# Performance work log

Measured on AMD Instinct MI355X. Metric: run time of the kernel, lower is better.

Reference implementation:

```python
import jax, jax.numpy as jnp
import numpy as np

EPS_NORM = 1e-12   # F.normalize eps
EPS_W = 1e-8       # weight eps in knn


def _l2_normalize(x):
    n = jnp.linalg.norm(x, axis=-1, keepdims=True)
    return x / jnp.maximum(n, EPS_NORM)


def setup_inputs() -> dict:
    key = jax.random.key(0)
    k1, k2, k3 = jax.random.split(key, 3)
    B, N, D, T = 2048, 100000, 128, 8
    return {
        "query": jax.random.normal(k1, (B, D), dtype=jnp.float32),
        "supports": jax.random.normal(k2, (N, D), dtype=jnp.float32),
        "targets": jax.random.uniform(k3, (N, T), dtype=jnp.float32),
        "k": 16,
    }


def reference(query, supports, targets, k):
    q = _l2_normalize(query)           # [B, D]
    s = _l2_normalize(supports)        # [N, D]
    dists = 1.0 - q @ s.T              # [B, N] cosine distance
    k = min(k, dists.shape[-1])
    # smallest-k distances == largest-k of negated distances
    neg_d, idx = jax.lax.top_k(-dists, k)   # [B, k]
    d = -neg_d
    w = 1.0 / (d + EPS_W)
    w = w / jnp.sum(w, axis=-1, keepdims=True)          # [B, k]
    tv = targets[idx]                                    # [B, k, T] gather
    return jnp.sum(tv * w[..., None], axis=1)            # [B, T]
```

## Files before the change

kernel.cpp:

```cpp
#include <hip/hip_runtime.h>


#define NSLICES 64
#define CN 64
#define BQ 128
#define NSUB 50
#define NGS (NSLICES * NSUB)
#define QCAP 64
#define THR_MARGIN 0.013f

typedef __bf16 bf16x8 __attribute__((ext_vector_type(8)));
typedef float f32x16 __attribute__((ext_vector_type(16)));

__device__ __forceinline__ ushort f2bf_rne(float f) {
  unsigned u = __float_as_uint(f);
  return (ushort)((u + 0x7FFFu + ((u >> 16) & 1u)) >> 16);
}
__device__ __forceinline__ ushort f2bf_down(float f) {
  unsigned u = __float_as_uint(f);
  return (ushort)((u >> 16) + (u >> 31));
}
__device__ __forceinline__ unsigned bf2key(ushort b) {
  return (unsigned)(b ^ ((b & 0x8000u) ? 0xFFFFu : 0x8000u));
}

__device__ __forceinline__ void bitonic64(float& v, unsigned& i, int lane) {
  #pragma unroll
  for (int k = 2; k <= 64; k <<= 1) {
    #pragma unroll
    for (int j = k >> 1; j > 0; j >>= 1) {
      float pv = __shfl_xor(v, j);
      unsigned pi = (unsigned)__shfl_xor((int)i, j);
      bool up = ((lane & k) == 0);
      bool lower = ((lane & j) == 0);
      bool gt = (v > pv) || (v == pv && i > pi);
      bool keep = (up == lower) ? !gt : gt;
      if (!keep) { v = pv; i = pi; }
    }
  }
}

__global__ __launch_bounds__(256) void norm_rows_k(
    const float* __restrict__ sup, const float* __restrict__ qry,
    ushort* __restrict__ sb, ushort* __restrict__ qb, int N, int nq) {
  int row = blockIdx.x * 4 + (threadIdx.x >> 6);
  int lane = threadIdx.x & 63;
  if (row >= N + nq) return;
  const float* src = (row < N) ? (sup + (size_t)row * 128)
                               : (qry + (size_t)(row - N) * 128);
  ushort* dst = (row < N) ? (sb + (size_t)row * 128)
                          : (qb + (size_t)(row - N) * 128);
  float2 v = *reinterpret_cast<const float2*>(src + lane * 2);
  float ss = v.x * v.x + v.y * v.y;
  #pragma unroll
  for (int o = 1; o < 64; o <<= 1) ss += __shfl_xor(ss, o);
  float inv = 1.0f / fmaxf(sqrtf(ss), 1e-12f);
  ushort2 h = make_ushort2(f2bf_rne(v.x * inv), f2bf_rne(v.y * inv));
  *reinterpret_cast<ushort2*>(dst + lane * 2) = h;
}

__device__ __forceinline__ void stage_lin(const ushort* __restrict__ sn,
                                          ushort* dst, int cb, int s1, int tid) {
  #pragma unroll
  for (int r = 0; r < 4; ++r) {
    int o = (r << 12) + tid * 16;
    int row = o >> 8;
    int dj = (o >> 4) & 15;
    int sj = dj ^ (row & 15);
    int srow = min(cb + row, s1 - 1);
    __builtin_amdgcn_global_load_lds(
        (const unsigned int*)(sn + (size_t)srow * 128 + sj * 8),
        (unsigned int*)(dst + (o >> 1)), 16, 0, 0);
  }
}

__device__ __forceinline__ void stage_list(const ushort* __restrict__ sn,
                                           ushort* dst, const ushort* slist_b,
                                           int s0, int s1, int tid) {
  #pragma unroll
  for (int r = 0; r < 4; ++r) {
    int o = (r << 12) + tid * 16;
    int row = o >> 8;
    int dj = (o >> 4) & 15;
    int sj = dj ^ (row & 15);
    int sub = slist_b[row >> 5];
    int lrow = (sub == 0xFFFF) ? 0 : sub * 32 + (row & 31);
    int srow = min(s0 + lrow, s1 - 1);
    __builtin_amdgcn_global_load_lds(
        (const unsigned int*)(sn + (size_t)srow * 128 + sj * 8),
        (unsigned int*)(dst + (o >> 1)), 16, 0, 0);
  }
}

__global__ __launch_bounds__(256, 4) void pass1_k(
    const ushort* __restrict__ qn, const ushort* __restrict__ sn,
    ushort* __restrict__ cm, int N) {
  __shared__ ushort st[2][CN * 128];
  const int tid = threadIdx.x;
  const int w = tid >> 6, lane = tid & 63;
  const int q32 = lane & 31, half = lane >> 5;
  const int L = blockIdx.x;
  const int xcd = L & 7, i6 = L >> 3;
  const int qtile = i6 & 15;
  const int slice = (xcd << 3) | (i6 >> 4);
  const int qbase = qtile * BQ;
  const int SLICE = (N + NSLICES - 1) / NSLICES;
  const int s0 = slice * SLICE;
  const int s1 = min(N, s0 + SLICE);
  const int nch = (s1 - s0 + CN - 1) / CN;

  stage_lin(sn, &st[0][0], s0, s1, tid);

  bf16x8 afr[8];
  {
    const int qrow = qbase + w * 32 + q32;
    #pragma unroll
    for (int t = 0; t < 8; ++t)
      afr[t] = *reinterpret_cast<const bf16x8*>(qn + (size_t)qrow * 128 + t * 16 + half * 8);
  }
  __syncthreads();

  int buf = 0;
  for (int ch = 0; ch < nch; ++ch) {
    const int cb = s0 + ch * CN;
    if (ch + 1 < nch) stage_lin(sn, &st[buf ^ 1][0], cb + CN, s1, tid);
    const ushort* stc = &st[buf][0];
    const bool lastch = (ch == nch - 1);

    f32x16 a0 = {0.f}, a1 = {0.f};
    #pragma unroll
    for (int r = 1; r < 16; ++r) { a0[r] = 0.f; a1[r] = 0.f; }
    const int r0 = q32;
    #pragma unroll
    for (int t = 0; t < 8; ++t) {
      int jb = t * 2 + half;
      int cj0 = jb ^ (r0 & 15);
      int cj1 = jb ^ ((r0 + 32) & 15);
      bf16x8 s0 = *reinterpret_cast<const bf16x8*>(&stc[r0 * 128 + cj0 * 8]);
      bf16x8 s1 = *reinterpret_cast<const bf16x8*>(&stc[(r0 + 32) * 128 + cj1 * 8]);
      a0 = __builtin_amdgcn_mfma_f32_32x32x16_bf16(s0, afr[t], a0, 0, 0, 0);
      a1 = __builtin_amdgcn_mfma_f32_32x32x16_bf16(s1, afr[t], a1, 0, 0, 0);
    }
    float v0 = -3.0e38f, v1 = -3.0e38f;
    if (lastch) {
      #pragma unroll
      for (int r = 0; r < 16; ++r) {
        int row = (r & 3) + 8 * (r >> 2) + (half << 2);
        if (cb + row < s1) v0 = fmaxf(v0, a0[r]);
        if (cb + 32 + row < s1) v1 = fmaxf(v1, a1[r]);
      }
    } else {
      #pragma unroll
      for (int r = 0; r < 16; ++r) {
        v0 = fmaxf(v0, a0[r]);
        v1 = fmaxf(v1, a1[r]);
      }
    }
    v0 = fmaxf(v0, __shfl_xor(v0, 32));
    v1 = fmaxf(v1, __shfl_xor(v1, 32));
    if (lane < 32) {
      int q = qbase + w * 32 + q32;
      size_t e0 = ((size_t)(q >> 2) * NGS + slice * NSUB + ch * 2) * 4 + (q & 3);
      cm[e0] = f2bf_down(v0);
      cm[e0 + 4] = f2bf_down(v1);
    }
    __syncthreads();
    buf ^= 1;
  }

  const int miss = NSUB - nch * 2;
  for (int idx = tid; idx < miss * BQ; idx += 256) {
    int sub = nch * 2 + idx / BQ;
    int q = qbase + (idx % BQ);
    cm[((size_t)(q >> 2) * NGS + (size_t)(slice * NSUB + sub)) * 4 + (q & 3)] = 0xFF80;
  }
}

__global__ __launch_bounds__(256) void thr_k(const ushort* __restrict__ cm,
                                             float* __restrict__ thr,
                                             unsigned* __restrict__ cnt) {
  const int q = blockIdx.x * 4 + (threadIdx.x >> 6);
  const int lane = threadIdx.x & 63;
  const size_t base = (size_t)(q >> 2) * NGS * 4 + (q & 3);
  unsigned keys[NGS / 128];
  #pragma unroll
  for (int j = 0; j < NGS / 128; ++j) {
    unsigned k0 = bf2key(cm[base + (size_t)(lane + 128 * j) * 4]);
    unsigned k1 = bf2key(cm[base + (size_t)(lane + 64 + 128 * j) * 4]);
    keys[j] = k0 | (k1 << 16);
  }
  unsigned res = 0;
  for (int b = 15; b >= 0; --b) {
    unsigned t = res | (1u << b);
    int c = 0;
    #pragma unroll
    for (int j = 0; j < NGS / 128; ++j)
      c += (int)((keys[j] & 0xFFFFu) >= t) + (int)((keys[j] >> 16) >= t);
    #pragma unroll
    for (int o = 1; o < 64; o <<= 1) c += __shfl_xor(c, o);
    if (c >= 16) res = t;
  }
  if (lane == 0) {
    ushort b16 = (ushort)((res & 0x8000u) ? (res ^ 0x8000u) : (res ^ 0xFFFFu));
    thr[q] = __uint_as_float((unsigned)b16 << 16) - THR_MARGIN;
    cnt[q] = 0;
  }
}

__global__ __launch_bounds__(256, 4) void pass2_k(
    const ushort* __restrict__ qn, const ushort* __restrict__ sn,
    const ushort* __restrict__ cm, const float* __restrict__ thr,
    unsigned* __restrict__ cnt, float2* __restrict__ candq, int N) {
  __shared__ ushort st[2][CN * 128];
  __shared__ float thr_l[BQ];
  __shared__ unsigned char hit[NSUB];
  __shared__ ushort slist[NSUB + 2];
  __shared__ int nhit_s;

  const int tid = threadIdx.x;
  const int w = tid >> 6, lane = tid & 63;
  const int q32 = lane & 31, half = lane >> 5;
  const int L = blockIdx.x;
  const int xcd = L & 7, i6 = L >> 3;
  const int qtile = i6 & 15;
  const int slice = (xcd << 3) | (i6 >> 4);
  const int qbase = qtile * BQ;
  const int SLICE = (N + NSLICES - 1) / NSLICES;
  const int s0 = slice * SLICE;
  const int s1 = min(N, s0 + SLICE);
  const int slen = s1 - s0;

  if (tid < BQ) thr_l[tid] = thr[qbase + tid];
  if (tid < NSUB) hit[tid] = 0;
  __syncthreads();

  {
    int q = qbase + (tid & 127);
    int sh = tid >> 7;
    float tq = thr_l[tid & 127];
    size_t base = (size_t)(q >> 2) * NGS * 4 + (q & 3);
    for (int j = 0; j < NSUB / 2; ++j) {
      int s = 2 * j + sh;
      ushort b = cm[base + (size_t)(slice * NSUB + s) * 4];
      if (__uint_as_float((unsigned)b << 16) >= tq) hit[s] = 1;
    }
  }
  __syncthreads();
  if (tid < 64) {
    bool f = (tid < NSUB) && hit[tid];
    unsigned long long bm = __ballot(f);
    int pos = __popcll(bm & ((1ull << tid) - 1ull));
    if (f) slist[pos] = (ushort)tid;
    if (tid == 0) {
      int total = __popcll(bm);
      nhit_s = total;
      slist[total] = 0xFFFF;
      slist[total + 1] = 0xFFFF;
    }
  }
  __syncthreads();
  const int nhit = nhit_s;
  if (nhit == 0) return;
  const int nb = (nhit + 1) >> 1;

  bf16x8 afr[8];
  {
    const int qrow = qbase + w * 32 + q32;
    #pragma unroll
    for (int t = 0; t < 8; ++t)
      afr[t] = *reinterpret_cast<const bf16x8*>(qn + (size_t)qrow * 128 + t * 16 + half * 8);
  }
  const float thrq = thr_l[w * 32 + q32];

  stage_list(sn, &st[0][0], &slist[0], s0, s1, tid);
  __syncthreads();

  int buf = 0;
  for (int b = 0; b < nb; ++b) {
    if (b + 1 < nb) stage_list(sn, &st[buf ^ 1][0], &slist[(b + 1) * 2], s0, s1, tid);
    const ushort* stc = &st[buf][0];

    f32x16 a0 = {0.f}, a1 = {0.f};
    #pragma unroll
    for (int r = 1; r < 16; ++r) { a0[r] = 0.f; a1[r] = 0.f; }
    const int r0 = q32;
    #pragma unroll
    for (int t = 0; t < 8; ++t) {
      int jb = t * 2 + half;
      int cj = jb ^ (r0 & 15);
      bf16x8 sf0 = *reinterpret_cast<const bf16x8*>(&stc[r0 * 128 + cj * 8]);
      bf16x8 sf1 = *reinterpret_cast<const bf16x8*>(&stc[(r0 + 32) * 128 + cj * 8]);
      a0 = __builtin_amdgcn_mfma_f32_32x32x16_bf16(sf0, afr[t], a0, 0, 0, 0);
      a1 = __builtin_amdgcn_mfma_f32_32x32x16_bf16(sf1, afr[t], a1, 0, 0, 0);
    }
    const int subA = slist[b * 2], subB = slist[b * 2 + 1];
    const int q = qbase + w * 32 + q32;
    if (subA != 0xFFFF) {
      unsigned hm = 0;
      #pragma unroll
      for (int r = 0; r < 16; ++r) {
        int row = (r & 3) + 8 * (r >> 2) + (half << 2);
        if (subA * 32 + row < slen && a0[r] >= thrq) hm |= 1u << r;
      }
      if (__any(hm != 0u)) {
        #pragma unroll
        for (int r = 0; r < 16; ++r) {
          if (hm & (1u << r)) {
            int row = (r & 3) + 8 * (r >> 2) + (half << 2);
            unsigned p = atomicAdd(&cnt[q], 1u);
            if (p < (unsigned)QCAP)
              candq[(size_t)q * QCAP + p] =
                  make_float2(a0[r], __int_as_float(s0 + subA * 32 + row));
          }
        }
      }
    }
    if (subB != 0xFFFF) {
      unsigned hm = 0;
      #pragma unroll
      for (int r = 0; r < 16; ++r) {
        int row = (r & 3) + 8 * (r >> 2) + (half << 2);
        if (subB * 32 + row < slen && a1[r] >= thrq) hm |= 1u << r;
      }
      if (__any(hm != 0u)) {
        #pragma unroll
        for (int r = 0; r < 16; ++r) {
          if (hm & (1u << r)) {
            int row = (r & 3) + 8 * (r >> 2) + (half << 2);
            unsigned p = atomicAdd(&cnt[q], 1u);
            if (p < (unsigned)QCAP)
              candq[(size_t)q * QCAP + p] =
                  make_float2(a1[r], __int_as_float(s0 + subB * 32 + row));
          }
        }
      }
    }
    __syncthreads();
    buf ^= 1;
  }
}

__global__ __launch_bounds__(256) void merge_refine_k(
    const float* __restrict__ query, const float* __restrict__ supports,
    const float* __restrict__ targets, const unsigned* __restrict__ cnt,
    const float2* __restrict__ candq, float* __restrict__ out) {
  const int W = threadIdx.x >> 6;
  const int q = blockIdx.x * 4 + W;
  const int lane = threadIdx.x & 63;
  __shared__ float qh_s[4][128];
  __shared__ float2 list[4][QCAP];
  __shared__ float2 refd[4][QCAP];

  int total = min((int)cnt[q], QCAP);
  if (lane < total) list[W][lane] = candq[(size_t)q * QCAP + lane];

  float2 qv = *reinterpret_cast<const float2*>(query + (size_t)q * 128 + lane * 2);
  double qss = (double)qv.x * qv.x + (double)qv.y * qv.y;
  #pragma unroll
  for (int o = 1; o < 64; o <<= 1) qss += __shfl_xor(qss, o);
  float qn1 = fmaxf((float)sqrt(qss), 1e-12f);
  qh_s[W][lane * 2] = qv.x / qn1;
  qh_s[W][lane * 2 + 1] = qv.y / qn1;
  __syncthreads();

  const int g16 = lane >> 4, m16 = lane & 15;
  float qh[8];
  #pragma unroll
  for (int d = 0; d < 8; ++d) qh[d] = qh_s[W][m16 * 8 + d];
  int rounds = (total + 3) >> 2;
  for (int r = 0; r < rounds; ++r) {
    int cc = r * 4 + g16;
    bool valid = cc < total;
    float2 ce = valid ? list[W][cc] : make_float2(0.f, __int_as_float(0));
    int sidx = __float_as_int(ce.y);
    float4 sa = *reinterpret_cast<const float4*>(supports + (size_t)sidx * 128 + m16 * 8);
    float4 sb = *reinterpret_cast<const float4*>(supports + (size_t)sidx * 128 + m16 * 8 + 4);
    float sv[8] = {sa.x, sa.y, sa.z, sa.w, sb.x, sb.y, sb.z, sb.w};
    double ss = 0.0, dt = 0.0;
    #pragma unroll
    for (int d = 0; d < 8; ++d) {
      ss += (double)sv[d] * sv[d];
      dt += (double)qh[d] * sv[d];
    }
    #pragma unroll
    for (int o = 1; o < 16; o <<= 1) {
      ss += __shfl_xor(ss, o);
      dt += __shfl_xor(dt, o);
    }
    if (m16 == 0 && valid) {
      float sn1 = fmaxf((float)sqrt(ss), 1e-12f);
      refd[W][cc] = make_float2((float)(1.0 - dt / (double)sn1), ce.y);
    }
  }
  __syncthreads();

  float dv = (lane < total) ? refd[W][lane].x : 3.0e38f;
  unsigned di = (lane < total) ? (unsigned)__float_as_int(refd[W][lane].y) : 0xFFFFFFFFu;
  bitonic64(dv, di, lane);

  float wv = (lane < 16) ? 1.0f / (dv + 1e-8f) : 0.0f;
  float wsum = wv;
  #pragma unroll
  for (int o = 1; o < 64; o <<= 1) wsum += __shfl_xor(wsum, o);
  float acc[8];
  #pragma unroll
  for (int t = 0; t < 8; ++t) acc[t] = 0.f;
  if (lane < 16) {
    float wn = wv / wsum;
    const float* tp = targets + (size_t)di * 8;
    #pragma unroll
    for (int t = 0; t < 8; ++t) acc[t] = wn * tp[t];
  }
  #pragma unroll
  for (int o = 1; o < 16; o <<= 1) {
    #pragma unroll
    for (int t = 0; t < 8; ++t) acc[t] += __shfl_xor(acc[t], o);
  }
  if (lane == 0) {
    #pragma unroll
    for (int t = 0; t < 8; ++t) out[(size_t)q * 8 + t] = acc[t];
  }
}

extern "C" void kernel_launch(void* const* d_in, const int* in_sizes, int n_in,
                              void* d_out, int out_size, void* d_ws, size_t ws_size,
                              hipStream_t stream) {
  const float* query = (const float*)d_in[0];
  const float* supports = (const float*)d_in[1];
  const float* targets = (const float*)d_in[2];
  float* out = (float*)d_out;
  const int D = 128;
  const int B = in_sizes[0] / D;
  const int N = in_sizes[1] / D;

  char* ws = (char*)d_ws;
  size_t off = 0;
  ushort* sn = (ushort*)(ws + off); off += (size_t)N * D * 2;
  off = (off + 255) & ~(size_t)255;
  ushort* qn = (ushort*)(ws + off); off += (size_t)B * D * 2;
  off = (off + 255) & ~(size_t)255;
  ushort* cm = (ushort*)(ws + off); off += (size_t)B * NGS * 2;
  off = (off + 255) & ~(size_t)255;
  float* thr = (float*)(ws + off); off += (size_t)B * 4;
  off = (off + 255) & ~(size_t)255;
  unsigned* cnt = (unsigned*)(ws + off); off += (size_t)B * 4;
  off = (off + 255) & ~(size_t)255;
  float2* candq = (float2*)(ws + off); off += (size_t)B * QCAP * sizeof(float2);
  if (off > ws_size) return;

  hipLaunchKernelGGL(norm_rows_k, dim3((N + B + 3) / 4), dim3(256), 0, stream,
                     supports, query, sn, qn, N, B);
  int nblk = (B / BQ) * NSLICES;
  hipLaunchKernelGGL(pass1_k, dim3(nblk), dim3(256), 0, stream, qn, sn, cm, N);
  hipLaunchKernelGGL(thr_k, dim3(B / 4), dim3(256), 0, stream, cm, thr, cnt);
  hipLaunchKernelGGL(pass2_k, dim3(nblk), dim3(256), 0, stream, qn, sn, cm, thr, cnt, candq, N);
  hipLaunchKernelGGL(merge_refine_k, dim3(B / 4), dim3(256), 0, stream, query, supports, targets, cnt, candq, out);
}
```

Baseline: 174.2 us.

## Halve candidate sub-group size to 16 rows for finer pruning

Pass 1 now records a bf16 max per 16-row sub-group instead of per 32-row sub-group, which doubles NSUB and the size of the coarse-max table. The top-16 threshold is still taken from those maxima, and pass 2 builds its hit list from 16-row groups, staging four groups per 64-row tile. The aim is a tighter threshold and fewer support rows run through MFMA and candidate emission in pass 2. In exchange, the coarse-max writes and reads double, thr_k holds twice as many keys per lane, and the hit-list compaction needs two ballot rounds.

Result: slower. 196.1 us (+12.6%).

```diff
diff --git a/kernel.cpp b/kernel.cpp
--- a/kernel.cpp
+++ b/kernel.cpp
@@ -4,7 +4,7 @@
 #define NSLICES 64
 #define CN 64
 #define BQ 128
-#define NSUB 50
+#define NSUB 100
 #define NGS (NSLICES * NSUB)
 #define QCAP 64
 #define THR_MARGIN 0.013f
@@ -83,8 +83,8 @@
     int row = o >> 8;
     int dj = (o >> 4) & 15;
     int sj = dj ^ (row & 15);
-    int sub = slist_b[row >> 5];
-    int lrow = (sub == 0xFFFF) ? 0 : sub * 32 + (row & 31);
+    int sub = slist_b[row >> 4];
+    int lrow = (sub == 0xFFFF) ? 0 : sub * 16 + (row & 15);
     int srow = min(s0 + lrow, s1 - 1);
     __builtin_amdgcn_global_load_lds(
         (const unsigned int*)(sn + (size_t)srow * 128 + sj * 8),
@@ -134,43 +134,41 @@
     #pragma unroll
     for (int t = 0; t < 8; ++t) {
       int jb = t * 2 + half;
-      int cj0 = jb ^ (r0 & 15);
-      int cj1 = jb ^ ((r0 + 32) & 15);
-      bf16x8 s0 = *reinterpret_cast<const bf16x8*>(&stc[r0 * 128 + cj0 * 8]);
-      bf16x8 s1 = *reinterpret_cast<const bf16x8*>(&stc[(r0 + 32) * 128 + cj1 * 8]);
-      a0 = __builtin_amdgcn_mfma_f32_32x32x16_bf16(s0, afr[t], a0, 0, 0, 0);
-      a1 = __builtin_amdgcn_mfma_f32_32x32x16_bf16(s1, afr[t], a1, 0, 0, 0);
-    }
-    float v0 = -3.0e38f, v1 = -3.0e38f;
-    if (lastch) {
-      #pragma unroll
-      for (int r = 0; r < 16; ++r) {
-        int row = (r & 3) + 8 * (r >> 2) + (half << 2);
-        if (cb + row < s1) v0 = fmaxf(v0, a0[r]);
-        if (cb + 32 + row < s1) v1 = fmaxf(v1, a1[r]);
-      }
-    } else {
-      #pragma unroll
-      for (int r = 0; r < 16; ++r) {
-        v0 = fmaxf(v0, a0[r]);
-        v1 = fmaxf(v1, a1[r]);
-      }
-    }
-    v0 = fmaxf(v0, __shfl_xor(v0, 32));
-    v1 = fmaxf(v1, __shfl_xor(v1, 32));
+      int cj = jb ^ (r0 & 15);
+      bf16x8 sf0 = *reinterpret_cast<const bf16x8*>(&stc[r0 * 128 + cj * 8]);
+      bf16x8 sf1 = *reinterpret_cast<const bf16x8*>(&stc[(r0 + 32) * 128 + cj * 8]);
+      a0 = __builtin_amdgcn_mfma_f32_32x32x16_bf16(sf0, afr[t], a0, 0, 0, 0);
+      a1 = __builtin_amdgcn_mfma_f32_32x32x16_bf16(sf1, afr[t], a1, 0, 0, 0);
+    }
+    float v0lo = -3.0e38f, v0hi = -3.0e38f, v1lo = -3.0e38f, v1hi = -3.0e38f;
+    #pragma unroll
+    for (int r = 0; r < 8; ++r) {
+      int row = (r & 3) + 8 * (r >> 2) + (half << 2);
+      int rowh = row + 16;
+      if (!lastch || cb + row < s1) v0lo = fmaxf(v0lo, a0[r]);
+      if (!lastch || cb + rowh < s1) v0hi = fmaxf(v0hi, a0[r + 8]);
+      if (!lastch || cb + 32 + row < s1) v1lo = fmaxf(v1lo, a1[r]);
+      if (!lastch || cb + 32 + rowh < s1) v1hi = fmaxf(v1hi, a1[r + 8]);
+    }
+    v0lo = fmaxf(v0lo, __shfl_xor(v0lo, 32));
+    v0hi = fmaxf(v0hi, __shfl_xor(v0hi, 32));
+    v1lo = fmaxf(v1lo, __shfl_xor(v1lo, 32));
+    v1hi = fmaxf(v1hi, __shfl_xor(v1hi, 32));
     if (lane < 32) {
       int q = qbase + w * 32 + q32;
-      size_t e0 = ((size_t)(q >> 2) * NGS + slice * NSUB + ch * 2) * 4 + (q & 3);
-      cm[e0] = f2bf_down(v0);
-      cm[e0 + 4] = f2bf_down(v1);
+      size_t e0 = ((size_t)(q >> 2) * NGS + slice * NSUB + ch * 4) * 4 + (q & 3);
+      cm[e0] = f2bf_down(v0lo);
+      cm[e0 + 4] = f2bf_down(v0hi);
+      cm[e0 + 8] = f2bf_down(v1lo);
+      cm[e0 + 12] = f2bf_down(v1hi);
     }
     __syncthreads();
     buf ^= 1;
   }
 
-  const int miss = NSUB - nch * 2;
+  const int miss = NSUB - nch * 4;
   for (int idx = tid; idx < miss * BQ; idx += 256) {
-    int sub = nch * 2 + idx / BQ;
+    int sub = nch * 4 + idx / BQ;
     int q = qbase + (idx % BQ);
     cm[((size_t)(q >> 2) * NGS + (size_t)(slice * NSUB + sub)) * 4 + (q & 3)] = 0xFF80;
   }
@@ -214,7 +212,7 @@
   __shared__ ushort st[2][CN * 128];
   __shared__ float thr_l[BQ];
   __shared__ unsigned char hit[NSUB];
-  __shared__ ushort slist[NSUB + 2];
+  __shared__ ushort slist[NSUB + 4];
   __shared__ int nhit_s;
 
   const int tid = threadIdx.x;
@@ -247,21 +245,26 @@
   }
   __syncthreads();
   if (tid < 64) {
-    bool f = (tid < NSUB) && hit[tid];
-    unsigned long long bm = __ballot(f);
-    int pos = __popcll(bm & ((1ull << tid) - 1ull));
-    if (f) slist[pos] = (ushort)tid;
+    int total = 0;
+    #pragma unroll
+    for (int r = 0; r < 2; ++r) {
+      int idx = r * 64 + tid;
+      bool f = (idx < NSUB) && hit[idx];
+      unsigned long long bm = __ballot(f);
+      int pos = total + __popcll(bm & ((1ull << tid) - 1ull));
+      if (f) slist[pos] = (ushort)idx;
+      total += __popcll(bm);
+    }
     if (tid == 0) {
-      int total = __popcll(bm);
       nhit_s = total;
-      slist[total] = 0xFFFF;
-      slist[total + 1] = 0xFFFF;
+      #pragma unroll
+      for (int p = 0; p < 4; ++p) slist[total + p] = 0xFFFF;
     }
   }
   __syncthreads();
   const int nhit = nhit_s;
   if (nhit == 0) return;
-  const int nb = (nhit + 1) >> 1;
+  const int nb = (nhit + 3) >> 2;
 
   bf16x8 afr[8];
   {
@@ -277,7 +280,7 @@
 
   int buf = 0;
   for (int b = 0; b < nb; ++b) {
-    if (b + 1 < nb) stage_list(sn, &st[buf ^ 1][0], &slist[(b + 1) * 2], s0, s1, tid);
+    if (b + 1 < nb) stage_list(sn, &st[buf ^ 1][0], &slist[(b + 1) * 4], s0, s1, tid);
     const ushort* stc = &st[buf][0];
 
     f32x16 a0 = {0.f}, a1 = {0.f};
@@ -293,44 +296,30 @@
       a0 = __builtin_amdgcn_mfma_f32_32x32x16_bf16(sf0, afr[t], a0, 0, 0, 0);
       a1 = __builtin_amdgcn_mfma_f32_32x32x16_bf16(sf1, afr[t], a1, 0, 0, 0);
     }
-    const int subA = slist[b * 2], subB = slist[b * 2 + 1];
     const int q = qbase + w * 32 + q32;
-    if (subA != 0xFFFF) {
+    #pragma unroll
+    for (int tile = 0; tile < 2; ++tile) {
       unsigned hm = 0;
       #pragma unroll
       for (int r = 0; r < 16; ++r) {
         int row = (r & 3) + 8 * (r >> 2) + (half << 2);
-        if (subA * 32 + row < slen && a0[r] >= thrq) hm |= 1u << r;
+        int sub = slist[b * 4 + tile * 2 + (row >> 4)];
+        int lrow = row & 15;
+        float sc = tile ? a1[r] : a0[r];
+        if (sub != 0xFFFF && sub * 16 + lrow < slen && sc >= thrq) hm |= 1u << r;
       }
       if (__any(hm != 0u)) {
         #pragma unroll
         for (int r = 0; r < 16; ++r) {
           if (hm & (1u << r)) {
             int row = (r & 3) + 8 * (r >> 2) + (half << 2);
+            int sub = slist[b * 4 + tile * 2 + (row >> 4)];
+            int lrow = row & 15;
+            float sc = tile ? a1[r] : a0[r];
             unsigned p = atomicAdd(&cnt[q], 1u);
             if (p < (unsigned)QCAP)
               candq[(size_t)q * QCAP + p] =
-                  make_float2(a0[r], __int_as_float(s0 + subA * 32 + row));
-          }
-        }
-      }
-    }
-    if (subB != 0xFFFF) {
-      unsigned hm = 0;
-      #pragma unroll
-      for (int r = 0; r < 16; ++r) {
-        int row = (r & 3) + 8 * (r >> 2) + (half << 2);
-        if (subB * 32 + row < slen && a1[r] >= thrq) hm |= 1u << r;
-      }
-      if (__any(hm != 0u)) {
-        #pragma unroll
-        for (int r = 0; r < 16; ++r) {
-          if (hm & (1u << r)) {
-            int row = (r & 3) + 8 * (r >> 2) + (half << 2);
-            unsigned p = atomicAdd(&cnt[q], 1u);
-            if (p < (unsigned)QCAP)
-              candq[(size_t)q * QCAP + p] =
-                  make_float2(a1[r], __int_as_float(s0 + subB * 32 + row));
+                  make_float2(sc, __int_as_float(s0 + sub * 16 + lrow));
           }
         }
       }
```
